# Performance work log

Measured on AMD Instinct MI355X. Metric: run time of the kernel, lower is better.

## Reference

```python
import jax, jax.numpy as jnp
import numpy as np
import math

B, T = 32, 64
VOCAB = 50005
EMB = 512
HID = 1024
SES = 1024
KNOW = 8785
NEG = math.exp(-100)

def _glorot(key, shape):
    fan_in, fan_out = shape[1], shape[0]
    lim = (6.0 / (fan_in + fan_out)) ** 0.5
    return jax.random.uniform(key, shape, jnp.float32, -lim, lim)

def setup_inputs() -> dict:
    key = jax.random.key(0)
    ks = jax.random.split(key, 16)
    inp = {}
    inp['ses_encoding'] = jax.random.normal(ks[0], (B, 1, SES), jnp.float32)
    inp['know_encoding'] = jax.random.normal(ks[1], (B, 1, SES), jnp.float32)
    inp['target'] = jax.random.randint(ks[2], (B, T), 0, 50000)
    inp['embed_w'] = jax.random.normal(ks[3], (VOCAB, EMB), jnp.float32) * 0.02
    # GRU params (PyTorch layout: W_ih [3H, E], W_hh [3H, H], gate order r,z,n)
    s = 1.0 / (HID ** 0.5)
    inp['W_ih'] = jax.random.uniform(ks[4], (3 * HID, EMB), jnp.float32, -s, s)
    inp['W_hh'] = jax.random.uniform(ks[5], (3 * HID, HID), jnp.float32, -s, s)
    inp['b_ih'] = jax.random.uniform(ks[6], (3 * HID,), jnp.float32, -s, s)
    inp['b_hh'] = jax.random.uniform(ks[7], (3 * HID,), jnp.float32, -s, s)
    inp['ses_to_dec_w'] = _glorot(ks[8], (HID, SES))
    inp['ses_to_dec_b'] = jnp.zeros((HID,), jnp.float32)
    inp['dec_inf_w'] = _glorot(ks[9], (2 * EMB, HID))
    inp['ses_inf_w'] = _glorot(ks[10], (2 * EMB, SES))
    inp['emb_inf_w'] = _glorot(ks[11], (2 * EMB, EMB))
    inp['emb_inf_b'] = jnp.zeros((2 * EMB,), jnp.float32)
    inp['W1'] = jax.random.normal(ks[12], (VOCAB, SES), jnp.float32) * 0.02
    inp['W2'] = jax.random.normal(ks[13], (VOCAB, SES), jnp.float32) * 0.02
    inp['W3'] = jax.random.normal(ks[14], (VOCAB, 2 * EMB), jnp.float32) * 0.02
    inp['W4'] = jax.random.normal(ks[15], (VOCAB, EMB), jnp.float32) * 0.02
    inp['know_vote_w'] = _glorot(jax.random.fold_in(key, 99), (KNOW, SES))
    return inp

def _gru_step(x, h, W_ih, W_hh, b_ih, b_hh):
    # x: [B,E], h: [B,H]
    gi = x @ W_ih.T + b_ih
    gh = h @ W_hh.T + b_hh
    ir, iz, inn = jnp.split(gi, 3, axis=-1)
    hr, hz, hn = jnp.split(gh, 3, axis=-1)
    r = jax.nn.sigmoid(ir + hr)
    z = jax.nn.sigmoid(iz + hz)
    n = jnp.tanh(inn + r * hn)
    return (1.0 - z) * h + z * n  # torch: h' = (1-z)*n + z*h with torch z; note torch formula

def _gru_step_torch(x, h, W_ih, W_hh, b_ih, b_hh):
    gi = x @ W_ih.T + b_ih
    gh = h @ W_hh.T + b_hh
    ir, iz, inn = jnp.split(gi, 3, axis=-1)
    hr, hz, hn = jnp.split(gh, 3, axis=-1)
    r = jax.nn.sigmoid(ir + hr)
    z = jax.nn.sigmoid(iz + hz)
    n = jnp.tanh(inn + r * hn)
    return (1.0 - z) * n + z * h

def reference(ses_encoding, know_encoding, target, embed_w, W_ih, W_hh, b_ih, b_hh,
              ses_to_dec_w, ses_to_dec_b, dec_inf_w, ses_inf_w, emb_inf_w, emb_inf_b,
              W1, W2, W3, W4, know_vote_w):
    ses = ses_encoding[:, 0, :]    # [B, SES]
    know = know_encoding[:, 0, :]  # [B, SES]
    target_emb = embed_w[target]   # [B, T, E]

    h0 = jnp.tanh(ses @ ses_to_dec_w.T + ses_to_dec_b)  # [B, H]

    # time-invariant pieces
    ses_inf_vec = ses @ ses_inf_w.T                      # [B, 2E]
    l1 = ses @ W1.T                                      # [B, V]
    l2 = know @ W2.T                                     # [B, V]
    # knowledge mixture log-probs (constant over time)
    ks = know @ know_vote_w.T                            # [B, KNOW]
    ks = ks[:, :-1]                                      # drop last -> [B, KNOW-1]
    pad_l = jnp.full((ks.shape[0], 10), NEG, ks.dtype)
    pad_r = jnp.full((ks.shape[0], VOCAB - 10 - (KNOW - 1)), NEG, ks.dtype)
    know_scores = jnp.concatenate([pad_l, ks, pad_r], axis=1)  # [B, V]
    know_probs = jax.nn.log_softmax(know_scores, axis=-1)      # [B, V]
    gate_const = l1 + l2                                 # [B, V]

    def step(h, emb_t):
        # emb_t: [B, E]
        h_new = _gru_step_torch(emb_t, h, W_ih, W_hh, b_ih, b_hh)  # [B, H]
        dec_hid_vec = h_new @ dec_inf_w.T                          # [B, 2E]
        target_inf = emb_t @ emb_inf_w.T + emb_inf_b               # [B, 2E]
        total = dec_hid_vec + ses_inf_vec + target_inf             # [B, 2E]
        mx = jnp.max(total.reshape(total.shape[0], EMB, 2), axis=-1)  # maxout -> [B, E]
        logits = mx @ embed_w.T                                    # shared embedding -> [B, V]
        hid_probs = jax.nn.log_softmax(logits, axis=-1)
        l3 = h_new @ W3.T                                          # note: W3 applied to hid_o [B,H]... but W3 is [V,2E]
        l4 = emb_t @ W4.T                                          # [B, V]
        gate = jax.nn.sigmoid(gate_const + l3 + l4)                # [B, V]
        final = gate * hid_probs + (1.0 - gate) * know_probs       # [B, V]
        return h_new, final

    # target_emb time-major for scan
    _, outs = jax.lax.scan(step, h0, jnp.swapaxes(target_emb, 0, 1))
    final_scores_all = jnp.swapaxes(outs, 0, 1)  # [B, T, V]
    return final_scores_all
```

## Files before the change

### kernel.cpp

```cpp
#include <hip/hip_runtime.h>

constexpr int VOC  = 50005;
constexpr int VOCP = 50048;
constexpr int VOCP2= 50176;
constexpr int NTM  = 391;
constexpr int NTMP = 400;
constexpr int KSN  = 8784;
constexpr float NPAD = 41221.0f;

typedef unsigned short u16;
typedef __attribute__((ext_vector_type(4))) float f32x4;
typedef __attribute__((ext_vector_type(8))) short bf16x8;

__device__ __forceinline__ float dot4(float4 a, float4 b) {
    return a.x*b.x + a.y*b.y + a.z*b.z + a.w*b.w;
}
__device__ __forceinline__ float sigmoidf_(float x) { return 1.0f / (1.0f + expf(-x)); }
__device__ __forceinline__ u16 f2bf(float f) {
    unsigned x = __float_as_uint(f);
    return (u16)((x + 0x7FFFu + ((x >> 16) & 1u)) >> 16);
}
__device__ __forceinline__ float bf2f(u16 u) { return __uint_as_float(((unsigned)u) << 16); }
__device__ __forceinline__ bf16x8 pack8(float4 lo, float4 hi) {
    union { bf16x8 v; unsigned u[4]; } r;
    r.u[0] = f2bf(lo.x) | ((unsigned)f2bf(lo.y) << 16);
    r.u[1] = f2bf(lo.z) | ((unsigned)f2bf(lo.w) << 16);
    r.u[2] = f2bf(hi.x) | ((unsigned)f2bf(hi.y) << 16);
    r.u[3] = f2bf(hi.z) | ((unsigned)f2bf(hi.w) << 16);
    return r.v;
}
template<int AUX>
__device__ __forceinline__ void gload_lds16x(const void* g, void* l) {
    __builtin_amdgcn_global_load_lds((const __attribute__((address_space(1))) unsigned int*)g,
                                     (__attribute__((address_space(3))) unsigned int*)l, 16, 0, AUX);
}
__device__ __forceinline__ void gload_lds16(const void* g, void* l) { gload_lds16x<0>(g, l); }
__device__ __forceinline__ void store_u16_sc(u16* p, u16 v) {
    asm volatile("global_store_short %0, %1, off sc0 sc1" :: "v"(p), "v"((unsigned)v) : "memory");
}
__device__ __forceinline__ void cvt4(const float* src, u16* dst) {
    float4 v = *(const float4*)src;
    unsigned lo = f2bf(v.x) | ((unsigned)f2bf(v.y) << 16);
    unsigned hi = f2bf(v.z) | ((unsigned)f2bf(v.w) << 16);
    *(uint2*)dst = make_uint2(lo, hi);
}
__device__ __forceinline__ void cvt64(const float* src, u16* dst) {
    float4 a = *(const float4*)src;
    float4 b = *(const float4*)(src + 4);
    float4 c = *(const float4*)(src + 8);
    float4 d = *(const float4*)(src + 12);
    uint2 pa = make_uint2(f2bf(a.x) | ((unsigned)f2bf(a.y) << 16), f2bf(a.z) | ((unsigned)f2bf(a.w) << 16));
    uint2 pb = make_uint2(f2bf(b.x) | ((unsigned)f2bf(b.y) << 16), f2bf(b.z) | ((unsigned)f2bf(b.w) << 16));
    uint2 pc = make_uint2(f2bf(c.x) | ((unsigned)f2bf(c.y) << 16), f2bf(c.z) | ((unsigned)f2bf(c.w) << 16));
    uint2 pd = make_uint2(f2bf(d.x) | ((unsigned)f2bf(d.y) << 16), f2bf(d.z) | ((unsigned)f2bf(d.w) << 16));
    *(uint2*)dst = pa; *(uint2*)(dst + 4) = pb; *(uint2*)(dst + 8) = pc; *(uint2*)(dst + 12) = pd;
}

template<int MODE>
__device__ void sk32_task(int task, int tid,
                          const float* __restrict__ A1, const float* __restrict__ A2,
                          const u16* __restrict__ Bsk, float* __restrict__ outp) {
    const int lane = tid & 63;
    const int w4 = tid >> 6;
    const int lrow = lane & 15;
    const int kg = lane >> 4;
    constexpr int K = (MODE == 0) ? 2048 : 1024;
    constexpr int bc0 = (MODE == 0) ? 0 : 1024;
    const int rowmax = (MODE == 0) ? (VOC - 1) : (KSN - 1);
    const int vb = task * 128 + w4 * 32;
    const int r0 = min(vb + lrow, rowmax);
    const int r1 = min(vb + 16 + lrow, rowmax);
    f32x4 acc[2][2] = {{{0.f,0.f,0.f,0.f},{0.f,0.f,0.f,0.f}},
                       {{0.f,0.f,0.f,0.f},{0.f,0.f,0.f,0.f}}};
    for (int k0 = 0; k0 < K; k0 += 32) {
        int kc = k0 + kg * 8;
        const float* s0;
        const float* s1;
        if (MODE == 0 && k0 >= 1024) {
            s0 = A2 + (size_t)r0 * 1024 + (kc - 1024);
            s1 = A2 + (size_t)r1 * 1024 + (kc - 1024);
        } else {
            s0 = A1 + (size_t)r0 * 1024 + kc;
            s1 = A1 + (size_t)r1 * 1024 + kc;
        }
        bf16x8 af0 = pack8(*(const float4*)s0, *(const float4*)(s0 + 4));
        bf16x8 af1 = pack8(*(const float4*)s1, *(const float4*)(s1 + 4));
        bf16x8 b0 = *(const bf16x8*)(Bsk + (size_t)lrow * 2048 + bc0 + kc);
        bf16x8 b1 = *(const bf16x8*)(Bsk + (size_t)(16 + lrow) * 2048 + bc0 + kc);
// ... 26 lines not shown

__global__ __launch_bounds__(256) void k_bsk(const float* __restrict__ ses,
                                             const float* __restrict__ know,
                                             u16* __restrict__ Bsk) {
    int row = blockIdx.x;
    for (int c0 = threadIdx.x * 4; c0 < 2048; c0 += 1024) {
        uint2 val = make_uint2(0, 0);
        if (row < 32) {
            const float* srcp = (c0 < 1024) ? ses + (size_t)row * 1024 + c0
                                            : know + (size_t)row * 1024 + (c0 - 1024);
            float4 v = *(const float4*)srcp;
            val = make_uint2(f2bf(v.x) | ((unsigned)f2bf(v.y) << 16),
                             f2bf(v.z) | ((unsigned)f2bf(v.w) << 16));
        }
        *(uint2*)(Bsk + (size_t)row * 2048 + c0) = val;
    }
}

__global__ __launch_bounds__(128) void k_gather(const float* __restrict__ embed,
                                                const int* __restrict__ target,
                                                u16* __restrict__ BG) {
    int n = blockIdx.x;
    int row = target[n];
    int c = threadIdx.x * 4;
    cvt4(embed + (size_t)row * 512 + c, BG + (size_t)n * 1536 + 1024 + c);
}

__global__ __launch_bounds__(256) void k_h0_sesinf(const float* __restrict__ ses,
                                                   const float* __restrict__ sdw,
                                                   const float* __restrict__ sdb,
                                                   const float* __restrict__ siw,
                                                   float* __restrict__ h0,
                                                   float* __restrict__ sesinf) {
    int g = blockIdx.x * 256 + threadIdx.x;
    int b = g & 31;
    int jg = g >> 5;
    int j0 = jg * 4;
    const float4* s4 = (const float4*)(ses + (size_t)b * 1024);
    const float4* wa[4];
    const float4* wc[4];
#pragma unroll
    for (int r = 0; r < 4; ++r) {
        wa[r] = (const float4*)(sdw + (size_t)(j0 + r) * 1024);
        wc[r] = (const float4*)(siw + (size_t)(j0 + r) * 1024);
    }
    float a[4] = {0, 0, 0, 0}, c[4] = {0, 0, 0, 0};
    for (int kq = 0; kq < 256; ++kq) {
        float4 sv = s4[kq];
#pragma unroll
        for (int r = 0; r < 4; ++r) { a[r] += dot4(sv, wa[r][kq]); c[r] += dot4(sv, wc[r][kq]); }
    }
#pragma unroll
    for (int r = 0; r < 4; ++r) {
        h0[b * 1024 + j0 + r] = tanhf(a[r] + sdb[j0 + r]);
        sesinf[b * 1024 + j0 + r] = c[r];
    }
}

__global__ __launch_bounds__(256) void k_lseknow(const float* __restrict__ ks,
                                                 float* __restrict__ lsek) {
    int b = blockIdx.x;
    int t = threadIdx.x;
    __shared__ float sm[256];
    float m = -1e30f;
    for (int j = t; j < KSN; j += 256) m = fmaxf(m, ks[(size_t)b * KSN + j]);
    sm[t] = m;
    __syncthreads();
    for (int s = 128; s > 0; s >>= 1) { if (t < s) sm[t] = fmaxf(sm[t], sm[t + s]); __syncthreads(); }
    m = fmaxf(sm[0], 0.0f);
    __syncthreads();
    float s = 0.0f;
    for (int j = t; j < KSN; j += 256) s += expf(ks[(size_t)b * KSN + j] - m);
    sm[t] = s;
    __syncthreads();
    for (int r = 128; r > 0; r >>= 1) { if (t < r) sm[t] += sm[t + r]; __syncthreads(); }
    if (t == 0) lsek[b] = m + logf(sm[0] + NPAD * expf(0.0f - m));
}

template<int EPI>
__global__ __launch_bounds__(256) void gemm_bt(
    const u16* __restrict__ A, int lda,
    const u16* __restrict__ B, int ldb, int K,
    const float* __restrict__ p0, const float* __restrict__ p1,
    float* __restrict__ q0, u16* __restrict__ q1, float* __restrict__ q3)
{
    __shared__ u16 Asm[128 * 64];
    __shared__ u16 Bsm[128 * 64];
    const int tid = threadIdx.x;
    const int lane = tid & 63;
    const int w = tid >> 6;
    const int wm = w >> 1, wn = w & 1;
    const int nt = blockIdx.x, mt = blockIdx.y;

    f32x4 acc[4][4];
#pragma unroll
    for (int i = 0; i < 4; ++i)
#pragma unroll
        for (int j = 0; j < 4; ++j) acc[i][j] = (f32x4){0.f, 0.f, 0.f, 0.f};

    for (int kt = 0; kt < K; kt += 64) {
#pragma unroll
        for (int p = 0; p < 4; ++p) {
            int flat = (w * 4 + p) * 64 + lane;
            int row = flat >> 3, slot = flat & 7;
            int ss = slot ^ (row & 7);
            gload_lds16(A + (size_t)(mt * 128 + row) * lda + kt + ss * 8, Asm + flat * 8);
            gload_lds16(B + (size_t)(nt * 128 + row) * ldb + kt + ss * 8, Bsm + flat * 8);
        }
        __syncthreads();
#pragma unroll
        for (int kc = 0; kc < 2; ++kc) {
            bf16x8 af[4], bfr[4];
#pragma unroll
            for (int mi = 0; mi < 4; ++mi) {
                int row = wm * 64 + mi * 16 + (lane & 15);
                int bcol = kc * 64 + ((lane >> 4) << 4);
                af[mi] = *(const bf16x8*)((const char*)Asm + row * 128 + (bcol ^ ((row & 7) << 4)));
            }
#pragma unroll
            for (int ni = 0; ni < 4; ++ni) {
                int row = wn * 64 + ni * 16 + (lane & 15);
                int bcol = kc * 64 + ((lane >> 4) << 4);
                bfr[ni] = *(const bf16x8*)((const char*)Bsm + row * 128 + (bcol ^ ((row & 7) << 4)));
            }
#pragma unroll
            for (int mi = 0; mi < 4; ++mi)
#pragma unroll
                for (int ni = 0; ni < 4; ++ni)
                    acc[mi][ni] = __builtin_amdgcn_mfma_f32_16x16x32_bf16(af[mi], bfr[ni], acc[mi][ni], 0, 0, 0);
        }
        __syncthreads();
    }

    const int cl = lane & 15;
    const int rg = (lane >> 4) << 2;

    if constexpr (EPI == 0) {
#pragma unroll
        for (int mi = 0; mi < 4; ++mi) {
            int m0 = mt * 128 + wm * 64 + mi * 16 + rg;
            float4 bias = *(const float4*)(p0 + m0);
#pragma unroll
            for (int ni = 0; ni < 4; ++ni) {
                int n = nt * 128 + wn * 64 + ni * 16 + cl;
                float4 v;
                v.x = acc[mi][ni][0] + bias.x; v.y = acc[mi][ni][1] + bias.y;
                v.z = acc[mi][ni][2] + bias.z; v.w = acc[mi][ni][3] + bias.w;
                *(float4*)(q0 + (size_t)n * 3072 + m0) = v;
            }
        }
    }
    if constexpr (EPI == 1) {
#pragma unroll
        for (int mi = 0; mi < 4; ++mi) {
            int m0 = mt * 128 + wm * 64 + mi * 16 + rg;
            float4 eb4 = *(const float4*)(p1 + m0);
#pragma unroll
            for (int ni = 0; ni < 4; ++ni) {
                int n = nt * 128 + wn * 64 + ni * 16 + cl;
                int b = n >> 6;
                float v0 = acc[mi][ni][0] + p0[b * 1024 + m0 + 0] + eb4.x;
                float v1 = acc[mi][ni][1] + p0[b * 1024 + m0 + 1] + eb4.y;
                float v2 = acc[mi][ni][2] + p0[b * 1024 + m0 + 2] + eb4.z;
                float v3 = acc[mi][ni][3] + p0[b * 1024 + m0 + 3] + eb4.w;
                unsigned pk = f2bf(fmaxf(v0, v1)) | ((unsigned)f2bf(fmaxf(v2, v3)) << 16);
                *(unsigned*)(q1 + (size_t)n * 512 + (m0 >> 1)) = pk;
            }
        }
    }
    if constexpr (EPI == 3) {
        __shared__ float redm[2][128];
        __shared__ float reds[2][128];
#pragma unroll
        for (int mi = 0; mi < 4; ++mi) {
            int v0 = mt * 128 + wm * 64 + mi * 16 + rg;
#pragma unroll
            for (int ni = 0; ni < 4; ++ni) {
                int n = nt * 128 + wn * 64 + ni * 16 + cl;
                unsigned lo = f2bf(acc[mi][ni][0]) | ((unsigned)f2bf(acc[mi][ni][1]) << 16);
                unsigned hi = f2bf(acc[mi][ni][2]) | ((unsigned)f2bf(acc[mi][ni][3]) << 16);
                *(uint2*)(q1 + (size_t)n * VOCP + v0) = make_uint2(lo, hi);
            }
        }
#pragma unroll
        for (int ni = 0; ni < 4; ++ni) {
            float lm = -1e30f;
#pragma unroll
            for (int mi = 0; mi < 4; ++mi) {
                int v0 = mt * 128 + wm * 64 + mi * 16 + rg;
#pragma unroll
                for (int r = 0; r < 4; ++r)
                    if (v0 + r < VOC) lm = fmaxf(lm, acc[mi][ni][r]);
            }
            lm = fmaxf(lm, __shfl_xor(lm, 16));
            lm = fmaxf(lm, __shfl_xor(lm, 32));
            float s = 0.0f;
#pragma unroll
            for (int mi = 0; mi < 4; ++mi) {
                int v0 = mt * 128 + wm * 64 + mi * 16 + rg;
#pragma unroll
                for (int r = 0; r < 4; ++r)
                    if (v0 + r < VOC) s += expf(acc[mi][ni][r] - lm);
            }
            s += __shfl_xor(s, 16);
            s += __shfl_xor(s, 32);
            if (lane < 16) {
                redm[wm][wn * 64 + ni * 16 + lane] = lm;
                reds[wm][wn * 64 + ni * 16 + lane] = s;
            }
        }
        __syncthreads();
        if (tid < 128) {
            float m0_ = redm[0][tid], m1_ = redm[1][tid];
            float m = fmaxf(m0_, m1_);
            float s = reds[0][tid] * expf(m0_ - m) + reds[1][tid] * expf(m1_ - m);
            int n = nt * 128 + tid;
            q0[(size_t)n * NTMP + mt] = m;
            q3[(size_t)n * NTMP + mt] = s;
        }
    }
}

__global__ __launch_bounds__(512, 1) void gemm_gate8(
    const u16* __restrict__ A,
    const u16* __restrict__ B,
    const float* __restrict__ gc2,
    unsigned char* __restrict__ g8)
{
    __shared__ __align__(16) char smem[131072];
    const int tid = threadIdx.x;
    const int lane = tid & 63;
    const int w = tid >> 6;
    const int wm = w >> 2;
    const int wn = w & 3;
    const int lrow = lane & 15;
    const int g = lane >> 4;

    int bid = blockIdx.x;
    int wg = (bid & 7) * 196 + (bid >> 3);
    int mt = wg >> 3;
    int nt = wg & 7;
    const size_t arow0 = (size_t)mt * 256;
    const size_t brow0 = (size_t)nt * 256;

    auto stageA = [&](int T, int h) {
        char* dst = smem + (T & 1) * 65536 + h * 16384;
        const u16* src = A + (arow0 + h * 128) * 1536 + T * 64;
#pragma unroll
        for (int q = 0; q < 2; ++q) {
            int flat = q * 512 + tid;
            int r = flat >> 3, s = flat & 7;
            int ss = s ^ (r & 7);
            gload_lds16(src + (size_t)r * 1536 + ss * 8, dst + flat * 16);
        }
    };
    auto stageB = [&](int T, int h) {
        char* dst = smem + (T & 1) * 65536 + 32768 + h * 16384;
        const u16* src = B + (brow0 + h * 128) * 1536 + T * 64;
#pragma unroll
        for (int q = 0; q < 2; ++q) {
            int flat = q * 512 + tid;
            int r = flat >> 3, s = flat & 7;
            int ss = s ^ (r & 7);
            gload_lds16(src + (size_t)r * 1536 + ss * 8, dst + flat * 16);
        }
    };

    f32x4 acc[8][4];
#pragma unroll
    for (int i = 0; i < 8; ++i)
#pragma unroll
        for (int j = 0; j < 4; ++j) acc[i][j] = (f32x4){0.f, 0.f, 0.f, 0.f};

    bf16x8 bf[4][2];
    auto loadB_ = [&](int d) {
        char* Bb = smem + d * 65536 + 32768 + (wn >> 1) * 16384;
#pragma unroll
        for (int ni = 0; ni < 4; ++ni) {
            int r = (wn & 1) * 64 + ni * 16 + lrow;
#pragma unroll
            for (int kk = 0; kk < 2; ++kk)
                bf[ni][kk] = *(const bf16x8*)(Bb + r * 128 + ((kk * 64 + g * 16) ^ ((r & 7) << 4)));
        }
    };

#define GPH2(D, Q, LB, STG)                                                           \
    {                                                                                 \
        STG;                                                                          \
        if (LB) loadB_(D);                                                            \
        bf16x8 af[2][2];                                                              \
        char* Ab = smem + (D) * 65536 + wm * 16384;                                   \
        _Pragma("unroll") for (int mi = 0; mi < 2; ++mi) {                            \
            int r = ((Q) * 2 + mi) * 16 + lrow;                                       \
            _Pragma("unroll") for (int kk = 0; kk < 2; ++kk)                          \
                af[mi][kk] = *(const bf16x8*)(Ab + r * 128 +                          \
                                ((kk * 64 + g * 16) ^ ((r & 7) << 4)));               \
        }                                                                             \
        asm volatile("s_waitcnt lgkmcnt(0)" ::: "memory");                            \
        __builtin_amdgcn_sched_barrier(0);                                            \
        __builtin_amdgcn_s_setprio(1);                                                \
        _Pragma("unroll") for (int kk = 0; kk < 2; ++kk)                              \
            _Pragma("unroll") for (int mi = 0; mi < 2; ++mi)                          \
                _Pragma("unroll") for (int ni = 0; ni < 4; ++ni)                      \
                    acc[(Q) * 2 + mi][ni] = __builtin_amdgcn_mfma_f32_16x16x32_bf16(  \
                        af[mi][kk], bf[ni][kk], acc[(Q) * 2 + mi][ni], 0, 0, 0);      \
        __builtin_amdgcn_s_setprio(0);                                                \
    }
#define BARR  __builtin_amdgcn_sched_barrier(0); __builtin_amdgcn_s_barrier(); \
              __builtin_amdgcn_sched_barrier(0)
#define VM4 asm volatile("s_waitcnt vmcnt(4)" ::: "memory"); __builtin_amdgcn_sched_barrier(0)
#define VM0 asm volatile("s_waitcnt vmcnt(0)" ::: "memory"); __builtin_amdgcn_sched_barrier(0)
#define NOPX (void)0

    stageB(0, 0); stageB(0, 1); stageA(0, 0); stageA(0, 1); stageB(1, 0); stageB(1, 1);
    VM4;
    BARR;

    for (int i = 0; i < 11; ++i) {
        int T0 = 2 * i, T1 = 2 * i + 1;
        GPH2(0, 0, true,  stageA(T1, 0));
        GPH2(0, 1, false, stageA(T1, 1));
        BARR;
        GPH2(0, 2, false, stageB(T0 + 2, 0));
        GPH2(0, 3, false, stageB(T0 + 2, 1));
        VM4; BARR;
        GPH2(1, 0, true,  stageA(T0 + 2, 0));
        GPH2(1, 1, false, stageA(T0 + 2, 1));
        BARR;
        GPH2(1, 2, false, stageB(T1 + 2, 0));
        GPH2(1, 3, false, stageB(T1 + 2, 1));
        VM4; BARR;
    }
    GPH2(0, 0, true,  stageA(23, 0));
    GPH2(0, 1, false, stageA(23, 1));
    BARR;
    GPH2(0, 2, false, NOPX);
    GPH2(0, 3, false, NOPX);
    VM0; BARR;
    GPH2(1, 0, true,  NOPX);
    GPH2(1, 1, false, NOPX);
    GPH2(1, 2, false, NOPX);
    GPH2(1, 3, false, NOPX);
#undef GPH2
#undef BARR
#undef VM4
#undef VM0
#undef NOPX

    const int rg = g << 2;
    const int b = nt * 4 + wn;
    const float* gcrow = gc2 + (size_t)b * VOCP2;
#pragma unroll
    for (int m = 0; m < 8; ++m) {
        int v0 = mt * 256 + wm * 128 + m * 16 + rg;
        float4 gcv = *(const float4*)(gcrow + v0);
#pragma unroll
        for (int ni = 0; ni < 4; ++ni) {
            int n = nt * 256 + wn * 64 + ni * 16 + lrow;
            unsigned pk = 0;
#pragma unroll
            for (int r = 0; r < 4; ++r) {
                float garg = acc[m][ni][r] + ((const float*)&gcv)[r];
                float gate = 1.0f / (1.0f + expf(-garg));
                pk |= ((unsigned)(int)(gate * 255.0f + 0.5f)) << (8 * r);
            }
            *(unsigned*)(g8 + (size_t)n * VOCP2 + v0) = pk;
        }
    }
}

__global__ __launch_bounds__(256, 1) void k_gru_f(const u16* __restrict__ WhhB,
                                                  const float* __restrict__ GI,
                                                  const float* __restrict__ bhh,
                                                  const u16* __restrict__ h0b,
                                                  u16* __restrict__ BG,
                                                  unsigned* __restrict__ flags,
                                                  const float* __restrict__ embed,
                                                  const float* __restrict__ W3,
                                                  const float* __restrict__ W4,
                                                  const float* __restrict__ dw,
                                                  const float* __restrict__ ew,
                                                  const float* __restrict__ W1,
                                                  const float* __restrict__ W2,
                                                  const float* __restrict__ kvw,
                                                  const u16* __restrict__ Bsk,
                                                  float* __restrict__ gc,
                                                  float* __restrict__ ksb,
                                                  u16* __restrict__ Aemb,
                                                  u16* __restrict__ A34,
                                                  u16* __restrict__ Adwew) {
    __shared__ __align__(16) char smem[163840];
    const int tid = threadIdx.x;

    if (blockIdx.x >= 64) {
        const int hb = blockIdx.x - 64;
        for (int t = hb; t < 392; t += 192) sk32_task<0>(t, tid, W1, W2, Bsk, gc);
        for (int t = hb; t < 69; t += 192) sk32_task<1>(t, tid, kvw, nullptr, Bsk, ksb);
        const long gtid = (long)hb * 256 + tid;
        const long gstr = 192L * 256;
        for (long i = gtid; i < (long)VOC * 32; i += gstr) {
            int row = (int)(i >> 5), c = ((int)i & 31) * 16;
            cvt64(embed + (size_t)row * 512 + c, Aemb + (size_t)row * 512 + c);
        }
        for (long i = gtid; i < (long)VOC * 64; i += gstr) {
            int row = (int)(i >> 6), c = ((int)i & 63) * 16;
            cvt64(W3 + (size_t)row * 1024 + c, A34 + (size_t)row * 1536 + c);
        }
        for (long i = gtid; i < (long)VOC * 32; i += gstr) {
            int row = (int)(i >> 5), c = ((int)i & 31) * 16;
            cvt64(W4 + (size_t)row * 512 + c, A34 + (size_t)row * 1536 + 1024 + c);
        }
        for (long i = gtid; i < 1024L * 64; i += gstr) {
            int row = (int)(i >> 6), c = ((int)i & 63) * 16;
            cvt64(dw + (size_t)row * 1024 + c, Adwew + (size_t)row * 1536 + c);
        }
        for (long i = gtid; i < 1024L * 32; i += gstr) {
            int row = (int)(i >> 5), c = ((int)i & 31) * 16;
            cvt64(ew + (size_t)row * 512 + c, Adwew + (size_t)row * 1536 + 1024 + c);
        }
        for (long i = gtid; i < (long)(VOCP2 - VOC) * 768; i += gstr) {
            int row = VOC + (int)(i / 768), c = (int)(i % 768);
            ((unsigned*)(A34 + (size_t)row * 1536))[c] = 0;
        }
        for (long i = gtid; i < (long)(VOCP - VOC) * 256; i += gstr) {
            int row = VOC + (int)(i >> 8), c = (int)i & 255;
            ((unsigned*)(Aemb + (size_t)row * 512))[c] = 0;
        }
        return;
    }

    const int lane = tid & 63;
    const int w = tid >> 6;
    const int jb = blockIdx.x;
    const int j0 = jb * 16;
    const int jl = tid & 15, bp = tid >> 4;
    const int je = j0 + jl;
    const float bh0 = bhh[je], bh1 = bhh[1024 + je], bh2 = bhh[2048 + je];
    char* Bbase = smem + 98304 + w * 16384;

#pragma unroll
    for (int it = 0; it < 24; ++it) {
        int flat = (it * 4 + w) * 64 + lane;
        int r = flat >> 7, s = flat & 127;
        int ss = s ^ (r & 7);
        int gr = (r >> 4) * 1024 + j0 + (r & 15);
        gload_lds16(WhhB + (size_t)gr * 1024 + ss * 8, smem + (size_t)flat * 16);
    }

    float hpv[2];
#pragma unroll
    for (int rb = 0; rb < 2; ++rb)
        hpv[rb] = bf2f(h0b[(size_t)(bp * 2 + rb) * 1024 + je]);

    const int lrow = lane & 15;
    const int ksel = lane >> 4;

    for (int t = 0; t < 64; ++t) {
        const u16* hsrc = (t == 0) ? h0b : BG + (size_t)(t - 1) * 1536;
        const size_t hstr = (t == 0) ? 1024 : (size_t)64 * 1536;

#pragma unroll
        for (int c = 0; c < 4; ++c) {
            char* dst = Bbase + c * 4096;
            int kq0 = w * 256 + c * 64;
#pragma unroll
            for (int q = 0; q < 4; ++q) {
                int flat = q * 64 + lane;
                int r = flat >> 3, s = flat & 7;
                int ss = s ^ (r & 7);
                gload_lds16x<0x11>(hsrc + (size_t)r * hstr + kq0 + ss * 8,
                                   dst + (size_t)flat * 16);
            }
        }
        float gi0[2], gi1[2], gi2[2];
#pragma unroll
        for (int rb = 0; rb < 2; ++rb) {
            const float* gp = GI + ((size_t)((bp * 2 + rb) * 64 + t)) * 3072 + je;
            gi0[rb] = gp[0]; gi1[rb] = gp[1024]; gi2[rb] = gp[2048];
        }
        if (t == 0) {
            __syncthreads();
        } else {
            asm volatile("s_waitcnt vmcnt(0)" ::: "memory");
        }
        __builtin_amdgcn_sched_barrier(0);

        f32x4 acc[3][2];
#pragma unroll
        for (int mi = 0; mi < 3; ++mi)
#pragma unroll
            for (int ni = 0; ni < 2; ++ni) acc[mi][ni] = (f32x4){0.f, 0.f, 0.f, 0.f};

#pragma unroll
        for (int c = 0; c < 4; ++c) {
            char* Bb = Bbase + c * 4096;
#pragma unroll
            for (int ks = 0; ks < 2; ++ks) {
                int kb = ks * 64 + ksel * 16;
                bf16x8 bfr[2];
#pragma unroll
                for (int ni = 0; ni < 2; ++ni) {
                    int br = ni * 16 + lrow;
                    bfr[ni] = *(const bf16x8*)(Bb + br * 128 + (kb ^ ((br & 7) << 4)));
                }
                int kA = w * 512 + c * 128 + kb;
#pragma unroll
                for (int mi = 0; mi < 3; ++mi) {
                    int ar = mi * 16 + lrow;
                    bf16x8 af = *(const bf16x8*)(smem + ar * 2048 + (kA ^ ((ar & 7) << 4)));
#pragma unroll
                    for (int ni = 0; ni < 2; ++ni)
                        acc[mi][ni] = __builtin_amdgcn_mfma_f32_16x16x32_bf16(af, bfr[ni], acc[mi][ni], 0, 0, 0);
                }
            }
        }

        float (*epiw)[33] = (float(*)[33])Bbase;
        asm volatile("s_waitcnt lgkmcnt(0)" ::: "memory");
        __builtin_amdgcn_sched_barrier(0);
        {
            const int rg = (lane >> 4) << 2;
#pragma unroll
            for (int mi = 0; mi < 3; ++mi)
#pragma unroll
                for (int ni = 0; ni < 2; ++ni) {
                    int m0 = mi * 16 + rg;
                    int cb = ni * 16 + lrow;
#pragma unroll
                    for (int r = 0; r < 4; ++r) epiw[m0 + r][cb] = acc[mi][ni][r];
                }
        }
        asm volatile("s_waitcnt lgkmcnt(0)" ::: "memory");
        __builtin_amdgcn_s_barrier();

#pragma unroll
        for (int rb = 0; rb < 2; ++rb) {
            int b = bp * 2 + rb;
            float s0 = 0.f, s1 = 0.f, s2 = 0.f;
#pragma unroll
            for (int ww = 0; ww < 4; ++ww) {
                float (*ep)[33] = (float(*)[33])(smem + 98304 + ww * 16384);
                s0 += ep[jl][b]; s1 += ep[16 + jl][b]; s2 += ep[32 + jl][b];
            }
            float rr = sigmoidf_(gi0[rb] + s0 + bh0);
            float zz = sigmoidf_(gi1[rb] + s1 + bh1);
            float nn = tanhf(gi2[rb] + rr * (s2 + bh2));
            float hnew = (1.0f - zz) * nn + zz * hpv[rb];
            hpv[rb] = hnew;
            store_u16_sc(BG + ((size_t)(b * 64 + t)) * 1536 + je, f2bf(hnew));
        }

        if (t < 63) {
            asm volatile("s_waitcnt vmcnt(0)" ::: "memory");
            __syncthreads();
            if (tid == 0)
                __hip_atomic_store(&flags[jb], (unsigned)(t + 1),
                                   __ATOMIC_RELAXED, __HIP_MEMORY_SCOPE_AGENT);
            unsigned tgt = (unsigned)(t + 1);
            while (true) {
                unsigned v = __hip_atomic_load(&flags[lane],
                                               __ATOMIC_RELAXED, __HIP_MEMORY_SCOPE_AGENT);
                if (__all(v >= tgt)) break;
                __builtin_amdgcn_s_sleep(1);
            }
            __builtin_amdgcn_sched_barrier(0);
        }
    }
}

__global__ __launch_bounds__(256) void k_lse(const float* __restrict__ pmax,
                                             const float* __restrict__ psum,
                                             float* __restrict__ lse) {
    int n = blockIdx.x;
    int t = threadIdx.x;
    __shared__ float sm[256];
    const float* pm = pmax + (size_t)n * NTMP;
    const float* ps = psum + (size_t)n * NTMP;
    float m = -1e30f;
    for (int p = t; p < NTM; p += 256) m = fmaxf(m, pm[p]);
    sm[t] = m;
    __syncthreads();
    for (int s = 128; s > 0; s >>= 1) { if (t < s) sm[t] = fmaxf(sm[t], sm[t + s]); __syncthreads(); }
    m = sm[0];
    __syncthreads();
    float s = 0.0f;
    for (int p = t; p < NTM; p += 256) s += ps[p] * expf(pm[p] - m);
    sm[t] = s;
    __syncthreads();
    for (int r = 128; r > 0; r >>= 1) { if (t < r) sm[t] += sm[t + r]; __syncthreads(); }
    if (t == 0) lse[n] = m + logf(sm[0]);
}

__global__ __launch_bounds__(256) void k_final(const u16* __restrict__ Lb,
                                               const unsigned char* __restrict__ g8,
                                               const float* __restrict__ lse,
                                               const float* __restrict__ ks,
                                               const float* __restrict__ lsek,
                                               float* __restrict__ out) {
    int n = blockIdx.y;
    int b = n >> 6;
    float lsen = lse[n], lkb = lsek[b];
    int base = blockIdx.x * 2048;
#pragma unroll
    for (int i = 0; i < 8; ++i) {
        int v = base + i * 256 + threadIdx.x;
        if (v < VOC) {
            float L = bf2f(Lb[(size_t)n * VOCP + v]);
            float g = g8[(size_t)n * VOCP2 + v] * (1.0f / 255.0f);
            float kp = ((v >= 10 && v < 10 + KSN) ? ks[(size_t)b * KSN + (v - 10)] : 0.0f) - lkb;
            out[(size_t)n * VOC + v] = g * (L - lsen) + (1.0f - g) * kp;
        }
    }
}

extern "C" void kernel_launch(void* const* d_in, const int* in_sizes, int n_in,
                              void* d_out, int out_size, void* d_ws, size_t ws_size,
                              hipStream_t stream) {
    const float* ses    = (const float*)d_in[0];
    const float* know   = (const float*)d_in[1];
    const int*   target = (const int*)d_in[2];
    const float* embed  = (const float*)d_in[3];
    const float* Wih    = (const float*)d_in[4];
    const float* Whh    = (const float*)d_in[5];
    const float* bih    = (const float*)d_in[6];
    const float* bhh    = (const float*)d_in[7];
    const float* sdw    = (const float*)d_in[8];
    const float* sdb    = (const float*)d_in[9];
    const float* dw     = (const float*)d_in[10];
    const float* siw    = (const float*)d_in[11];
    const float* ew     = (const float*)d_in[12];
    const float* eb     = (const float*)d_in[13];
    const float* W1     = (const float*)d_in[14];
    const float* W2     = (const float*)d_in[15];
    const float* W3     = (const float*)d_in[16];
    const float* W4     = (const float*)d_in[17];
    const float* kvw    = (const float*)d_in[18];

    char* ws = (char*)d_ws;
    size_t o = 0;
    auto alloc = [&](size_t bytes) { char* r = ws + o; o += (bytes + 255) & ~(size_t)255; return r; };
    u16*   Aemb  = (u16*)  alloc((size_t)VOCP * 512 * 2);
    u16*   A34   = (u16*)  alloc((size_t)VOCP2 * 1536 * 2);
    u16*   Adwew = (u16*)  alloc((size_t)1024 * 1536 * 2);
    u16*   Wihb  = (u16*)  alloc((size_t)3072 * 512 * 2);
    u16*   WhhB  = (u16*)  alloc((size_t)3072 * 1024 * 2);
    u16*   h0b   = (u16*)  alloc((size_t)32 * 1024 * 2);
    u16*   BG    = (u16*)  alloc((size_t)2048 * 1536 * 2);
    u16*   BL    = (u16*)  alloc((size_t)2048 * 512 * 2);
    float* GI    = (float*)alloc((size_t)2048 * 3072 * 4);
    float* h0    = (float*)alloc((size_t)32 * 1024 * 4);
    float* sesinf= (float*)alloc((size_t)32 * 1024 * 4);
    float* gc    = (float*)alloc((size_t)32 * VOCP2 * 4);
    float* ksb   = (float*)alloc((size_t)32 * KSN * 4);
    float* lsek  = (float*)alloc(256);
    float* lse   = (float*)alloc((size_t)2048 * 4);
    unsigned* flags = (unsigned*)alloc(256);
    float* pmax  = (float*)alloc((size_t)2048 * NTMP * 4);
    float* psum  = (float*)alloc((size_t)2048 * NTMP * 4);
    unsigned char* g8 = (unsigned char*)alloc((size_t)2048 * VOCP2);
    u16*   Lb    = (u16*)  alloc((size_t)2048 * VOCP * 2);
    u16*   Bsk   = (u16*)  alloc((size_t)128 * 2048 * 2);
    float* out = (float*)d_out;

    hipMemsetAsync(flags, 0, 256, stream);

    k_cvt<<<dim3(3072, 1), 256, 0, stream>>>(Wih, Wihb, 512, 512, 512);
    k_cvt<<<dim3(3072, 1), 256, 0, stream>>>(Whh, WhhB, 1024, 1024, 1024);
    k_bsk<<<dim3(128), 256, 0, stream>>>(ses, know, Bsk);
    k_gather<<<dim3(2048), 128, 0, stream>>>(embed, target, BG);
    k_h0_sesinf<<<dim3(32), 256, 0, stream>>>(ses, sdw, sdb, siw, h0, sesinf);
    k_cvt<<<dim3(32, 1), 256, 0, stream>>>(h0, h0b, 1024, 1024, 1024);

    gemm_bt<0><<<dim3(16, 24), 256, 0, stream>>>(Wihb, 512, BG + 1024, 1536, 512,
                                                 bih, nullptr, GI, nullptr, nullptr);
    k_gru_f<<<dim3(256), 256, 0, stream>>>(WhhB, GI, bhh, h0b, BG, flags,
                                           embed, W3, W4, dw, ew,
                                           W1, W2, kvw, Bsk, gc, ksb,
                                           Aemb, A34, Adwew);
    k_lseknow<<<dim3(32), 256, 0, stream>>>(ksb, lsek);
    gemm_bt<1><<<dim3(16, 8), 256, 0, stream>>>(Adwew, 1536, BG, 1536, 1536,
                                                sesinf, eb, nullptr, BL, nullptr);
    gemm_gate8<<<dim3(1568), 512, 0, stream>>>(A34, BG, gc, g8);
    gemm_bt<3><<<dim3(16, NTM), 256, 0, stream>>>(Aemb, 512, BL, 512, 512,
                                                  nullptr, nullptr, pmax, Lb, psum);
    k_lse<<<dim3(2048), 256, 0, stream>>>(pmax, psum, lse);
    k_final<<<dim3(25, 2048), 256, 0, stream>>>(Lb, g8, lse, ksb, lsek, out);
}
```

Baseline: 1.394 ms.

## Fuse final output combination into gate GEMM epilogue and drop g8 buffer

The gate GEMM epilogue now reads the bf16 logits, the row log-sum-exp and the knowledge scores, and writes the final mixed output directly. This removes the quantized 8-bit gate buffer round trip through memory and the separate final kernel. The gate GEMM is moved after the logsumexp kernel so that its inputs are ready. The epilogue's stores and Lb loads are strided across rows in small chunks, which may coalesce less well than the old streaming final kernel. Gate precision also improves because the 8-bit quantization is gone.

```diff
diff --git a/kernel.cpp b/kernel.cpp
--- a/kernel.cpp
+++ b/kernel.cpp
@@ -339,7 +339,11 @@
     const u16* __restrict__ A,
     const u16* __restrict__ B,
     const float* __restrict__ gc2,
-    unsigned char* __restrict__ g8)
+    const u16* __restrict__ Lb,
+    const float* __restrict__ lse,
+    const float* __restrict__ ks,
+    const float* __restrict__ lsek,
+    float* __restrict__ out)
 {
     __shared__ __align__(16) char smem[131072];
     const int tid = threadIdx.x;
@@ -464,21 +468,32 @@
     const int rg = g << 2;
     const int b = nt * 4 + wn;
     const float* gcrow = gc2 + (size_t)b * VOCP2;
-#pragma unroll
-    for (int m = 0; m < 8; ++m) {
-        int v0 = mt * 256 + wm * 128 + m * 16 + rg;
-        float4 gcv = *(const float4*)(gcrow + v0);
-#pragma unroll
-        for (int ni = 0; ni < 4; ++ni) {
-            int n = nt * 256 + wn * 64 + ni * 16 + lrow;
-            unsigned pk = 0;
+    const float lsekb = lsek[b];
+#pragma unroll
+    for (int ni = 0; ni < 4; ++ni) {
+        int n = nt * 256 + wn * 64 + ni * 16 + lrow;
+        float lsen = lse[n];
+#pragma unroll
+        for (int m = 0; m < 8; ++m) {
+            int v0 = mt * 256 + wm * 128 + m * 16 + rg;
+            if (v0 >= VOC) continue;
+            float4 gcv = *(const float4*)(gcrow + v0);
+            uint2 lb2 = *(const uint2*)(Lb + (size_t)n * VOCP + v0);
+            u16 lbs[4] = {(u16)(lb2.x & 0xffffu), (u16)(lb2.x >> 16),
+                          (u16)(lb2.y & 0xffffu), (u16)(lb2.y >> 16)};
+            float ov[4];
 #pragma unroll
             for (int r = 0; r < 4; ++r) {
                 float garg = acc[m][ni][r] + ((const float*)&gcv)[r];
                 float gate = 1.0f / (1.0f + expf(-garg));
-                pk |= ((unsigned)(int)(gate * 255.0f + 0.5f)) << (8 * r);
-            }
-            *(unsigned*)(g8 + (size_t)n * VOCP2 + v0) = pk;
+                float L = bf2f(lbs[r]);
+                int v = v0 + r;
+                float kp = ((v >= 10 && v < 10 + KSN) ? ks[(size_t)b * KSN + (v - 10)] : 0.0f) - lsekb;
+                ov[r] = gate * (L - lsen) + (1.0f - gate) * kp;
+            }
+#pragma unroll
+            for (int r = 0; r < 4; ++r)
+                if (v0 + r < VOC) out[(size_t)n * VOC + v0 + r] = ov[r];
         }
     }
 }
@@ -705,28 +720,6 @@
     if (t == 0) lse[n] = m + logf(sm[0]);
 }
 
-__global__ __launch_bounds__(256) void k_final(const u16* __restrict__ Lb,
-                                               const unsigned char* __restrict__ g8,
-                                               const float* __restrict__ lse,
-                                               const float* __restrict__ ks,
-                                               const float* __restrict__ lsek,
-                                               float* __restrict__ out) {
-    int n = blockIdx.y;
-    int b = n >> 6;
-    float lsen = lse[n], lkb = lsek[b];
-    int base = blockIdx.x * 2048;
-#pragma unroll
-    for (int i = 0; i < 8; ++i) {
-        int v = base + i * 256 + threadIdx.x;
-        if (v < VOC) {
-            float L = bf2f(Lb[(size_t)n * VOCP + v]);
-            float g = g8[(size_t)n * VOCP2 + v] * (1.0f / 255.0f);
-            float kp = ((v >= 10 && v < 10 + KSN) ? ks[(size_t)b * KSN + (v - 10)] : 0.0f) - lkb;
-            out[(size_t)n * VOC + v] = g * (L - lsen) + (1.0f - g) * kp;
-        }
-    }
-}
-
 extern "C" void kernel_launch(void* const* d_in, const int* in_sizes, int n_in,
                               void* d_out, int out_size, void* d_ws, size_t ws_size,
                               hipStream_t stream) {
@@ -771,7 +764,6 @@
     unsigned* flags = (unsigned*)alloc(256);
     float* pmax  = (float*)alloc((size_t)2048 * NTMP * 4);
     float* psum  = (float*)alloc((size_t)2048 * NTMP * 4);
-    unsigned char* g8 = (unsigned char*)alloc((size_t)2048 * VOCP2);
     u16*   Lb    = (u16*)  alloc((size_t)2048 * VOCP * 2);
     u16*   Bsk   = (u16*)  alloc((size_t)128 * 2048 * 2);
     float* out = (float*)d_out;
@@ -794,9 +786,8 @@
     k_lseknow<<<dim3(32), 256, 0, stream>>>(ksb, lsek);
     gemm_bt<1><<<dim3(16, 8), 256, 0, stream>>>(Adwew, 1536, BG, 1536, 1536,
                                                 sesinf, eb, nullptr, BL, nullptr);
-    gemm_gate8<<<dim3(1568), 512, 0, stream>>>(A34, BG, gc, g8);
     gemm_bt<3><<<dim3(16, NTM), 256, 0, stream>>>(Aemb, 512, BL, 512, 512,
                                                   nullptr, nullptr, pmax, Lb, psum);
     k_lse<<<dim3(2048), 256, 0, stream>>>(pmax, psum, lse);
-    k_final<<<dim3(25, 2048), 256, 0, stream>>>(Lb, g8, lse, ksb, lsek, out);
-}
+    gemm_gate8<<<dim3(1568), 512, 0, stream>>>(A34, BG, gc, Lb, lse, ksb, lsek, out);
+}
```

Measured after the change: 1.413 ms. Within noise of the previous version (+1.4%).

## Replace 128x128 logits GEMM with pipelined 256x256 tile kernel

Applied to the files above, without the earlier changes.

The vocabulary-logits GEMM (embedding weights times maxout output, K=512) moves from the generic 128x128-tile gemm_bt kernel to a new 512-thread, 256x256-tile kernel with double-buffered direct-to-LDS loads. This mirrors the existing gate GEMM and keeps the fused bf16 store plus per-tile max/sum partials. Vocab padding is widened to 50176 so tiles divide evenly, and the LSE reduction now handles 196 partials per row instead of 391. The aim is more data reuse and better MFMA pipelining, at the cost of higher register and LDS use per block.

```diff
diff --git a/kernel.cpp b/kernel.cpp
--- a/kernel.cpp
+++ b/kernel.cpp
@@ -1,9 +1,8 @@
 #include <hip/hip_runtime.h>
 
 constexpr int VOC  = 50005;
-constexpr int VOCP = 50048;
 constexpr int VOCP2= 50176;
-constexpr int NTM  = 391;
+constexpr int NT2  = 196;
 constexpr int NTMP = 400;
 constexpr int KSN  = 8784;
 constexpr float NPAD = 41221.0f;
@@ -196,7 +195,7 @@
     const u16* __restrict__ A, int lda,
     const u16* __restrict__ B, int ldb, int K,
     const float* __restrict__ p0, const float* __restrict__ p1,
-    float* __restrict__ q0, u16* __restrict__ q1, float* __restrict__ q3)
+    float* __restrict__ q0, u16* __restrict__ q1)
 {
     __shared__ u16 Asm[128 * 64];
     __shared__ u16 Bsm[128 * 64];
@@ -282,121 +281,7 @@
             }
         }
     }
-    if constexpr (EPI == 3) {
-        __shared__ float redm[2][128];
-        __shared__ float reds[2][128];
-#pragma unroll
-        for (int mi = 0; mi < 4; ++mi) {
-            int v0 = mt * 128 + wm * 64 + mi * 16 + rg;
-#pragma unroll
-            for (int ni = 0; ni < 4; ++ni) {
-                int n = nt * 128 + wn * 64 + ni * 16 + cl;
-                unsigned lo = f2bf(acc[mi][ni][0]) | ((unsigned)f2bf(acc[mi][ni][1]) << 16);
-                unsigned hi = f2bf(acc[mi][ni][2]) | ((unsigned)f2bf(acc[mi][ni][3]) << 16);
-                *(uint2*)(q1 + (size_t)n * VOCP + v0) = make_uint2(lo, hi);
-            }
-        }
-#pragma unroll
-        for (int ni = 0; ni < 4; ++ni) {
-            float lm = -1e30f;
-#pragma unroll
-            for (int mi = 0; mi < 4; ++mi) {
-                int v0 = mt * 128 + wm * 64 + mi * 16 + rg;
-#pragma unroll
-                for (int r = 0; r < 4; ++r)
-                    if (v0 + r < VOC) lm = fmaxf(lm, acc[mi][ni][r]);
-            }
-            lm = fmaxf(lm, __shfl_xor(lm, 16));
-            lm = fmaxf(lm, __shfl_xor(lm, 32));
-            float s = 0.0f;
-#pragma unroll
-            for (int mi = 0; mi < 4; ++mi) {
-                int v0 = mt * 128 + wm * 64 + mi * 16 + rg;
-#pragma unroll
-                for (int r = 0; r < 4; ++r)
-                    if (v0 + r < VOC) s += expf(acc[mi][ni][r] - lm);
-            }
-            s += __shfl_xor(s, 16);
-            s += __shfl_xor(s, 32);
-            if (lane < 16) {
-                redm[wm][wn * 64 + ni * 16 + lane] = lm;
-                reds[wm][wn * 64 + ni * 16 + lane] = s;
-            }
-        }
-        __syncthreads();
-        if (tid < 128) {
-            float m0_ = redm[0][tid], m1_ = redm[1][tid];
-            float m = fmaxf(m0_, m1_);
-            float s = reds[0][tid] * expf(m0_ - m) + reds[1][tid] * expf(m1_ - m);
-            int n = nt * 128 + tid;
-            q0[(size_t)n * NTMP + mt] = m;
-            q3[(size_t)n * NTMP + mt] = s;
-        }
-    }
-}
-
-__global__ __launch_bounds__(512, 1) void gemm_gate8(
-    const u16* __restrict__ A,
-    const u16* __restrict__ B,
-    const float* __restrict__ gc2,
-    unsigned char* __restrict__ g8)
-{
-    __shared__ __align__(16) char smem[131072];
-    const int tid = threadIdx.x;
-    const int lane = tid & 63;
-    const int w = tid >> 6;
-    const int wm = w >> 2;
-    const int wn = w & 3;
-    const int lrow = lane & 15;
-    const int g = lane >> 4;
-
-    int bid = blockIdx.x;
-    int wg = (bid & 7) * 196 + (bid >> 3);
-    int mt = wg >> 3;
-    int nt = wg & 7;
-    const size_t arow0 = (size_t)mt * 256;
-    const size_t brow0 = (size_t)nt * 256;
-
-    auto stageA = [&](int T, int h) {
-        char* dst = smem + (T & 1) * 65536 + h * 16384;
-        const u16* src = A + (arow0 + h * 128) * 1536 + T * 64;
-#pragma unroll
-        for (int q = 0; q < 2; ++q) {
-            int flat = q * 512 + tid;
-            int r = flat >> 3, s = flat & 7;
-            int ss = s ^ (r & 7);
-            gload_lds16(src + (size_t)r * 1536 + ss * 8, dst + flat * 16);
-        }
-    };
-    auto stageB = [&](int T, int h) {
-        char* dst = smem + (T & 1) * 65536 + 32768 + h * 16384;
-        const u16* src = B + (brow0 + h * 128) * 1536 + T * 64;
-#pragma unroll
-        for (int q = 0; q < 2; ++q) {
-            int flat = q * 512 + tid;
-            int r = flat >> 3, s = flat & 7;
-            int ss = s ^ (r & 7);
-            gload_lds16(src + (size_t)r * 1536 + ss * 8, dst + flat * 16);
-        }
-    };
-
-    f32x4 acc[8][4];
-#pragma unroll
-    for (int i = 0; i < 8; ++i)
-#pragma unroll
-        for (int j = 0; j < 4; ++j) acc[i][j] = (f32x4){0.f, 0.f, 0.f, 0.f};
-
-    bf16x8 bf[4][2];
-    auto loadB_ = [&](int d) {
-        char* Bb = smem + d * 65536 + 32768 + (wn >> 1) * 16384;
-#pragma unroll
-        for (int ni = 0; ni < 4; ++ni) {
-            int r = (wn & 1) * 64 + ni * 16 + lrow;
-#pragma unroll
-            for (int kk = 0; kk < 2; ++kk)
-                bf[ni][kk] = *(const bf16x8*)(Bb + r * 128 + ((kk * 64 + g * 16) ^ ((r & 7) << 4)));
-        }
-    };
+}
 
 #define GPH2(D, Q, LB, STG)                                                           \
     {                                                                                 \
@@ -426,9 +311,71 @@
 #define VM0 asm volatile("s_waitcnt vmcnt(0)" ::: "memory"); __builtin_amdgcn_sched_barrier(0)
 #define NOPX (void)0
 
+__global__ __launch_bounds__(512, 1) void gemm_gate8(
+    const u16* __restrict__ A,
+    const u16* __restrict__ B,
+    const float* __restrict__ gc2,
+    unsigned char* __restrict__ g8)
+{
+    __shared__ __align__(16) char smem[131072];
+    const int tid = threadIdx.x;
+    const int lane = tid & 63;
+    const int w = tid >> 6;
+    const int wm = w >> 2;
+    const int wn = w & 3;
+    const int lrow = lane & 15;
+    const int g = lane >> 4;
+
+    int bid = blockIdx.x;
+    int wg = (bid & 7) * 196 + (bid >> 3);
+    int mt = wg >> 3;
+    int nt = wg & 7;
+    const size_t arow0 = (size_t)mt * 256;
+    const size_t brow0 = (size_t)nt * 256;
+
+    auto stageA = [&](int T, int h) {
+        char* dst = smem + (T & 1) * 65536 + h * 16384;
+        const u16* src = A + (arow0 + h * 128) * 1536 + T * 64;
+#pragma unroll
+        for (int q = 0; q < 2; ++q) {
+            int flat = q * 512 + tid;
+            int r = flat >> 3, s = flat & 7;
+            int ss = s ^ (r & 7);
+            gload_lds16(src + (size_t)r * 1536 + ss * 8, dst + flat * 16);
+        }
+    };
+    auto stageB = [&](int T, int h) {
+        char* dst = smem + (T & 1) * 65536 + 32768 + h * 16384;
+        const u16* src = B + (brow0 + h * 128) * 1536 + T * 64;
+#pragma unroll
+        for (int q = 0; q < 2; ++q) {
+            int flat = q * 512 + tid;
+            int r = flat >> 3, s = flat & 7;
+            int ss = s ^ (r & 7);
+            gload_lds16(src + (size_t)r * 1536 + ss * 8, dst + flat * 16);
+        }
+    };
+
+    f32x4 acc[8][4];
+#pragma unroll
+    for (int i = 0; i < 8; ++i)
+#pragma unroll
+        for (int j = 0; j < 4; ++j) acc[i][j] = (f32x4){0.f, 0.f, 0.f, 0.f};
+
+    bf16x8 bf[4][2];
+    auto loadB_ = [&](int d) {
+        char* Bb = smem + d * 65536 + 32768 + (wn >> 1) * 16384;
+#pragma unroll
+        for (int ni = 0; ni < 4; ++ni) {
+            int r = (wn & 1) * 64 + ni * 16 + lrow;
+#pragma unroll
+            for (int kk = 0; kk < 2; ++kk)
+                bf[ni][kk] = *(const bf16x8*)(Bb + r * 128 + ((kk * 64 + g * 16) ^ ((r & 7) << 4)));
+        }
+    };
+
     stageB(0, 0); stageB(0, 1); stageA(0, 0); stageA(0, 1); stageB(1, 0); stageB(1, 1);
-    VM4;
-    BARR;
+    VM4; BARR;
 
     for (int i = 0; i < 11; ++i) {
         int T0 = 2 * i, T1 = 2 * i + 1;
@@ -455,33 +402,182 @@
     GPH2(1, 1, false, NOPX);
     GPH2(1, 2, false, NOPX);
     GPH2(1, 3, false, NOPX);
+
+    const int rg = g << 2;
+    const int b = nt * 4 + wn;
+    const float* gcrow = gc2 + (size_t)b * VOCP2;
+#pragma unroll
+    for (int m = 0; m < 8; ++m) {
+        int v0 = mt * 256 + wm * 128 + m * 16 + rg;
+        float4 gcv = *(const float4*)(gcrow + v0);
+#pragma unroll
+        for (int ni = 0; ni < 4; ++ni) {
+            int n = nt * 256 + wn * 64 + ni * 16 + lrow;
+            unsigned pk = 0;
+#pragma unroll
+            for (int r = 0; r < 4; ++r) {
+                float garg = acc[m][ni][r] + ((const float*)&gcv)[r];
+                float gate = 1.0f / (1.0f + expf(-garg));
+                pk |= ((unsigned)(int)(gate * 255.0f + 0.5f)) << (8 * r);
+            }
+            *(unsigned*)(g8 + (size_t)n * VOCP2 + v0) = pk;
+        }
+    }
+}
+
+__global__ __launch_bounds__(512, 1) void gemm_log8(
+    const u16* __restrict__ A,
+    const u16* __restrict__ B,
+    u16* __restrict__ Lb,
+    float* __restrict__ pmax,
+    float* __restrict__ psum)
+{
+    __shared__ __align__(16) char smem[131072];
+    const int tid = threadIdx.x;
+    const int lane = tid & 63;
+    const int w = tid >> 6;
+    const int wm = w >> 2;
+    const int wn = w & 3;
+    const int lrow = lane & 15;
+    const int g = lane >> 4;
+
+    int bid = blockIdx.x;
+    int wg = (bid & 7) * 196 + (bid >> 3);
+    int mt = wg >> 3;
+    int nt = wg & 7;
+    const size_t arow0 = (size_t)mt * 256;
+    const size_t brow0 = (size_t)nt * 256;
+
+    auto stageA = [&](int T, int h) {
+        char* dst = smem + (T & 1) * 65536 + h * 16384;
+        const u16* src = A + (arow0 + h * 128) * 512 + T * 64;
+#pragma unroll
+        for (int q = 0; q < 2; ++q) {
+            int flat = q * 512 + tid;
+            int r = flat >> 3, s = flat & 7;
+            int ss = s ^ (r & 7);
+            gload_lds16(src + (size_t)r * 512 + ss * 8, dst + flat * 16);
+        }
+    };
+    auto stageB = [&](int T, int h) {
+        char* dst = smem + (T & 1) * 65536 + 32768 + h * 16384;
+        const u16* src = B + (brow0 + h * 128) * 512 + T * 64;
+#pragma unroll
+        for (int q = 0; q < 2; ++q) {
+            int flat = q * 512 + tid;
+            int r = flat >> 3, s = flat & 7;
+            int ss = s ^ (r & 7);
+            gload_lds16(src + (size_t)r * 512 + ss * 8, dst + flat * 16);
+        }
+    };
+
+    f32x4 acc[8][4];
+#pragma unroll
+    for (int i = 0; i < 8; ++i)
+#pragma unroll
+        for (int j = 0; j < 4; ++j) acc[i][j] = (f32x4){0.f, 0.f, 0.f, 0.f};
+
+    bf16x8 bf[4][2];
+    auto loadB_ = [&](int d) {
+        char* Bb = smem + d * 65536 + 32768 + (wn >> 1) * 16384;
+#pragma unroll
+        for (int ni = 0; ni < 4; ++ni) {
+            int r = (wn & 1) * 64 + ni * 16 + lrow;
+#pragma unroll
+            for (int kk = 0; kk < 2; ++kk)
+                bf[ni][kk] = *(const bf16x8*)(Bb + r * 128 + ((kk * 64 + g * 16) ^ ((r & 7) << 4)));
+        }
+    };
+
+    stageB(0, 0); stageB(0, 1); stageA(0, 0); stageA(0, 1); stageB(1, 0); stageB(1, 1);
+    VM4; BARR;
+
+    for (int i = 0; i < 3; ++i) {
+        int T0 = 2 * i, T1 = 2 * i + 1;
+        GPH2(0, 0, true,  stageA(T1, 0));
+        GPH2(0, 1, false, stageA(T1, 1));
+        BARR;
+        GPH2(0, 2, false, stageB(T0 + 2, 0));
+        GPH2(0, 3, false, stageB(T0 + 2, 1));
+        VM4; BARR;
+        GPH2(1, 0, true,  stageA(T0 + 2, 0));
+        GPH2(1, 1, false, stageA(T0 + 2, 1));
+        BARR;
+        GPH2(1, 2, false, stageB(T1 + 2, 0));
+        GPH2(1, 3, false, stageB(T1 + 2, 1));
+        VM4; BARR;
+    }
+    GPH2(0, 0, true,  stageA(7, 0));
+    GPH2(0, 1, false, stageA(7, 1));
+    BARR;
+    GPH2(0, 2, false, NOPX);
+    GPH2(0, 3, false, NOPX);
+    VM0; BARR;
+    GPH2(1, 0, true,  NOPX);
+    GPH2(1, 1, false, NOPX);
+    GPH2(1, 2, false, NOPX);
+    GPH2(1, 3, false, NOPX);
+
+    BARR;
+    const int rg = g << 2;
+#pragma unroll
+    for (int m = 0; m < 8; ++m) {
+        int v0 = mt * 256 + wm * 128 + m * 16 + rg;
+#pragma unroll
+        for (int ni = 0; ni < 4; ++ni) {
+            int n = nt * 256 + wn * 64 + ni * 16 + lrow;
+            unsigned lo = f2bf(acc[m][ni][0]) | ((unsigned)f2bf(acc[m][ni][1]) << 16);
+            unsigned hi = f2bf(acc[m][ni][2]) | ((unsigned)f2bf(acc[m][ni][3]) << 16);
+            *(uint2*)(Lb + (size_t)n * VOCP2 + v0) = make_uint2(lo, hi);
+        }
+    }
+    {
+        float* redm = (float*)smem;
+        float* reds = (float*)(smem + 2048);
+#pragma unroll
+        for (int ni = 0; ni < 4; ++ni) {
+            float lm = -1e30f;
+#pragma unroll
+            for (int m = 0; m < 8; ++m) {
+                int v0 = mt * 256 + wm * 128 + m * 16 + rg;
+#pragma unroll
+                for (int r = 0; r < 4; ++r)
+                    if (v0 + r < VOC) lm = fmaxf(lm, acc[m][ni][r]);
+            }
+            lm = fmaxf(lm, __shfl_xor(lm, 16));
+            lm = fmaxf(lm, __shfl_xor(lm, 32));
+            float s = 0.0f;
+#pragma unroll
+            for (int m = 0; m < 8; ++m) {
+                int v0 = mt * 256 + wm * 128 + m * 16 + rg;
+#pragma unroll
+                for (int r = 0; r < 4; ++r)
+                    if (v0 + r < VOC) s += expf(acc[m][ni][r] - lm);
+            }
+            s += __shfl_xor(s, 16);
+            s += __shfl_xor(s, 32);
+            if (lane < 16) {
+                redm[wm * 256 + wn * 64 + ni * 16 + lane] = lm;
+                reds[wm * 256 + wn * 64 + ni * 16 + lane] = s;
+            }
+        }
+        asm volatile("s_waitcnt lgkmcnt(0)" ::: "memory");
+        BARR;
+        if (tid < 256) {
+            float m0_ = redm[tid], m1_ = redm[256 + tid];
+            float m = fmaxf(m0_, m1_);
+            float s = reds[tid] * expf(m0_ - m) + reds[256 + tid] * expf(m1_ - m);
+            int n = nt * 256 + tid;
+            pmax[(size_t)n * NTMP + mt] = m;
+            psum[(size_t)n * NTMP + mt] = s;
+        }
+    }
+}
 #undef GPH2
 #undef BARR
 #undef VM4
 #undef VM0
 #undef NOPX
-
-    const int rg = g << 2;
-    const int b = nt * 4 + wn;
-    const float* gcrow = gc2 + (size_t)b * VOCP2;
-#pragma unroll
-    for (int m = 0; m < 8; ++m) {
-        int v0 = mt * 256 + wm * 128 + m * 16 + rg;
-        float4 gcv = *(const float4*)(gcrow + v0);
-#pragma unroll
-        for (int ni = 0; ni < 4; ++ni) {
-            int n = nt * 256 + wn * 64 + ni * 16 + lrow;
-            unsigned pk = 0;
-#pragma unroll
-            for (int r = 0; r < 4; ++r) {
-                float garg = acc[m][ni][r] + ((const float*)&gcv)[r];
-                float gate = 1.0f / (1.0f + expf(-garg));
-                pk |= ((unsigned)(int)(gate * 255.0f + 0.5f)) << (8 * r);
-            }
-            *(unsigned*)(g8 + (size_t)n * VOCP2 + v0) = pk;
-        }
-    }
-}
 
 __global__ __launch_bounds__(256, 1) void k_gru_f(const u16* __restrict__ WhhB,
                                                   const float* __restrict__ GI,
@@ -536,7 +632,7 @@
             int row = VOC + (int)(i / 768), c = (int)(i % 768);
             ((unsigned*)(A34 + (size_t)row * 1536))[c] = 0;
         }
-        for (long i = gtid; i < (long)(VOCP - VOC) * 256; i += gstr) {
+        for (long i = gtid; i < (long)(VOCP2 - VOC) * 256; i += gstr) {
             int row = VOC + (int)(i >> 8), c = (int)i & 255;
             ((unsigned*)(Aemb + (size_t)row * 512))[c] = 0;
         }
@@ -691,14 +787,14 @@
     const float* pm = pmax + (size_t)n * NTMP;
     const float* ps = psum + (size_t)n * NTMP;
     float m = -1e30f;
-    for (int p = t; p < NTM; p += 256) m = fmaxf(m, pm[p]);
+    if (t < NT2) m = pm[t];
     sm[t] = m;
     __syncthreads();
     for (int s = 128; s > 0; s >>= 1) { if (t < s) sm[t] = fmaxf(sm[t], sm[t + s]); __syncthreads(); }
     m = sm[0];
     __syncthreads();
     float s = 0.0f;
-    for (int p = t; p < NTM; p += 256) s += ps[p] * expf(pm[p] - m);
+    if (t < NT2) s = ps[t] * expf(pm[t] - m);
     sm[t] = s;
     __syncthreads();
     for (int r = 128; r > 0; r >>= 1) { if (t < r) sm[t] += sm[t + r]; __syncthreads(); }
@@ -719,7 +815,7 @@
     for (int i = 0; i < 8; ++i) {
         int v = base + i * 256 + threadIdx.x;
         if (v < VOC) {
-            float L = bf2f(Lb[(size_t)n * VOCP + v]);
+            float L = bf2f(Lb[(size_t)n * VOCP2 + v]);
             float g = g8[(size_t)n * VOCP2 + v] * (1.0f / 255.0f);
             float kp = ((v >= 10 && v < 10 + KSN) ? ks[(size_t)b * KSN + (v - 10)] : 0.0f) - lkb;
             out[(size_t)n * VOC + v] = g * (L - lsen) + (1.0f - g) * kp;
@@ -753,7 +849,7 @@
     char* ws = (char*)d_ws;
     size_t o = 0;
     auto alloc = [&](size_t bytes) { char* r = ws + o; o += (bytes + 255) & ~(size_t)255; return r; };
-    u16*   Aemb  = (u16*)  alloc((size_t)VOCP * 512 * 2);
+    u16*   Aemb  = (u16*)  alloc((size_t)VOCP2 * 512 * 2);
     u16*   A34   = (u16*)  alloc((size_t)VOCP2 * 1536 * 2);
     u16*   Adwew = (u16*)  alloc((size_t)1024 * 1536 * 2);
     u16*   Wihb  = (u16*)  alloc((size_t)3072 * 512 * 2);
@@ -772,7 +868,7 @@
     float* pmax  = (float*)alloc((size_t)2048 * NTMP * 4);
     float* psum  = (float*)alloc((size_t)2048 * NTMP * 4);
     unsigned char* g8 = (unsigned char*)alloc((size_t)2048 * VOCP2);
-    u16*   Lb    = (u16*)  alloc((size_t)2048 * VOCP * 2);
+    u16*   Lb    = (u16*)  alloc((size_t)2048 * VOCP2 * 2);
     u16*   Bsk   = (u16*)  alloc((size_t)128 * 2048 * 2);
     float* out = (float*)d_out;
 
@@ -786,17 +882,16 @@
     k_cvt<<<dim3(32, 1), 256, 0, stream>>>(h0, h0b, 1024, 1024, 1024);
 
     gemm_bt<0><<<dim3(16, 24), 256, 0, stream>>>(Wihb, 512, BG + 1024, 1536, 512,
-                                                 bih, nullptr, GI, nullptr, nullptr);
+                                                 bih, nullptr, GI, nullptr);
     k_gru_f<<<dim3(256), 256, 0, stream>>>(WhhB, GI, bhh, h0b, BG, flags,
                                            embed, W3, W4, dw, ew,
                                            W1, W2, kvw, Bsk, gc, ksb,
                                            Aemb, A34, Adwew);
     k_lseknow<<<dim3(32), 256, 0, stream>>>(ksb, lsek);
     gemm_bt<1><<<dim3(16, 8), 256, 0, stream>>>(Adwew, 1536, BG, 1536, 1536,
-                                                sesinf, eb, nullptr, BL, nullptr);
+                                                sesinf, eb, nullptr, BL);
     gemm_gate8<<<dim3(1568), 512, 0, stream>>>(A34, BG, gc, g8);
-    gemm_bt<3><<<dim3(16, NTM), 256, 0, stream>>>(Aemb, 512, BL, 512, 512,
-                                                  nullptr, nullptr, pmax, Lb, psum);
+    gemm_log8<<<dim3(1568), 512, 0, stream>>>(Aemb, BL, Lb, pmax, psum);
     k_lse<<<dim3(2048), 256, 0, stream>>>(pmax, psum, lse);
     k_final<<<dim3(25, 2048), 256, 0, stream>>>(Lb, g8, lse, ksb, lsek, out);
 }
```

After: 1.407 ms. No clear change (+1.0%).
